# Kernel tuning notes

Measured on AMD Instinct MI355X. Metric: run time of the kernel, lower is better.

Reference implementation:

```python
import jax, jax.numpy as jnp
import numpy as np

N = 100000      # nodes
E = 1600000     # edges
IN, H1, H2, OUT = 128, 128, 64, 128  # layer_channel = [128, (128+128)//2, (128+128)//4, 128]


def setup_inputs() -> dict:
    key = jax.random.key(0)
    ks = jax.random.split(key, 11)
    w = lambda k, s: (jax.random.normal(k, s, jnp.float32) * 0.05)
    return {
        "x": jax.random.normal(ks[0], (N, IN), jnp.float32),
        "edge_index": jax.random.randint(ks[1], (2, E), 0, N),
        "gcn1_w": w(ks[2], (IN, H1)),   "gcn1_b": jnp.zeros((H1,), jnp.float32),
        "fc2_w": w(ks[3], (H1, H1)),   # nn.Linear weight [out, in]
        "gcn3_w": w(ks[4], (H1, H2)),   "gcn3_b": jnp.zeros((H2,), jnp.float32),
        "fc4_w": w(ks[5], (H2, H2)),
        "gcn5_w": w(ks[6], (H2, OUT)),  "gcn5_b": jnp.zeros((OUT,), jnp.float32),
        "fc6_w": w(ks[7], (OUT, OUT)),
    }


def _gcn_norm(edge_index):
    # PyG GCNConv default: add self-loops, symmetric normalization D^-1/2 (A+I) D^-1/2
    loop = jnp.arange(N, dtype=edge_index.dtype)
    src = jnp.concatenate([edge_index[0], loop])
    dst = jnp.concatenate([edge_index[1], loop])
    deg = jax.ops.segment_sum(jnp.ones_like(src, jnp.float32), dst, num_segments=N)
    dinv = jnp.where(deg > 0, jax.lax.rsqrt(jnp.maximum(deg, 1.0)), 0.0)
    norm = dinv[src] * dinv[dst]  # [E+N]
    return src, dst, norm


def _gcn_conv(x, W, b, src, dst, norm):
    h = x @ W                              # [N, d_out]
    msg = h[src] * norm[:, None]           # gather + scale over edges
    return jax.ops.segment_sum(msg, dst, num_segments=N) + b


def reference(x, edge_index, gcn1_w, gcn1_b, fc2_w, gcn3_w, gcn3_b, fc4_w, gcn5_w, gcn5_b, fc6_w):
    src, dst, norm = _gcn_norm(edge_index)
    relu = jax.nn.relu
    z1 = relu(_gcn_conv(x, gcn1_w, gcn1_b, src, dst, norm))
    z1 = relu(z1 + z1 @ fc2_w.T)
    z2 = relu(_gcn_conv(z1, gcn3_w, gcn3_b, src, dst, norm))
    z2 = relu(z2 + z2 @ fc4_w.T)
    z3 = relu(_gcn_conv(z2, gcn5_w, gcn5_b, src, dst, norm))
    z3 = relu(z3 + z3 @ fc6_w.T)
    return z3
```

## Files before the change

### kernel.cpp

```cpp
#include <hip/hip_runtime.h>
#include <cstdint>
#include <cstddef>

#define NN 100000
#define NE 1600000
#define NBB 391
#define BSTRIDE 5120

typedef short short8 __attribute__((ext_vector_type(8)));
typedef float floatx4 __attribute__((ext_vector_type(4)));
typedef unsigned short u16;
typedef uint32_t u32;

__device__ __forceinline__ void split_bf16(float f, short& hi, short& lo) {
    union { float f; uint32_t u; } x;
    x.f = f;
    uint32_t uh = x.u + 0x7FFFu + ((x.u >> 16) & 1u);
    hi = (short)(uh >> 16);
    union { uint32_t u; float f; } hf;
    hf.u = (uh >> 16) << 16;
    float r = f - hf.f;
    union { float f; uint32_t u; } y;
    y.f = r;
    uint32_t ul = y.u + 0x7FFFu + ((y.u >> 16) & 1u);
    lo = (short)(ul >> 16);
}

__device__ __forceinline__ u16 f2bf(float f) {
    union { float f; uint32_t u; } x;
    x.f = f;
    uint32_t r = x.u + 0x7FFFu + ((x.u >> 16) & 1u);
    return (u16)(r >> 16);
}

__device__ __forceinline__ float bf2f(u16 h) {
    union { uint32_t u; float f; } x;
    x.u = ((uint32_t)h) << 16;
    return x.f;
}

__device__ __forceinline__ void acc2(uint32_t u, float& a0, float& a1) {
    union { uint32_t u; float f; } lo, hi;
    lo.u = u << 16;
    hi.u = u & 0xFFFF0000u;
    a0 += lo.f;
    a1 += hi.f;
}

struct WDesc {
    const float* W;
    short* fh;
    short* fl;
    int din, dout, transb, base, total;
};
struct WPrepArgs { WDesc d[6]; int* gcur; };

static __global__ void k_wprep(WPrepArgs args) {
    int tid = blockIdx.x * 256 + threadIdx.x;
    if (tid <= NBB) args.gcur[tid] = 0;
#pragma unroll
    for (int i = 0; i < 6; i++) {
        const WDesc& D = args.d[i];
        if (tid >= D.base && tid < D.base + D.total) {
            int local = tid - D.base;
            int lane = local & 63;
            int rest = local >> 6;
            int kst = D.din >> 5;
            int ks = rest % kst;
            int ntile = rest / kst;
            int n = ntile * 16 + (lane & 15);
            int k0 = ks * 32 + (lane >> 4) * 8;
#pragma unroll
            for (int j = 0; j < 8; j++) {
                int k = k0 + j;
                float v = D.transb ? D.W[(size_t)n * D.din + k]
                                   : D.W[(size_t)k * D.dout + n];
                short h, l;
                split_bf16(v, h, l);
                D.fh[(size_t)local * 8 + j] = h;
                D.fl[(size_t)local * 8 + j] = l;
            }
        }
    }
}


static __global__ __launch_bounds__(1024) void k_bscatterF(const int* __restrict__ src,
                                                           const int* __restrict__ dst,
                                                           int* __restrict__ gcur,
                                                           int2* __restrict__ staging) {
    __shared__ int h[NBB + 1];
    __shared__ int base[NBB + 1];
    int t = threadIdx.x;
    for (int i = t; i < NBB; i += 1024) h[i] = 0;
    __syncthreads();
    int e0 = blockIdx.x * 4096;
    int b[4], l[4], sv[4], dv[4];
#pragma unroll
    for (int j = 0; j < 4; j++) {
        int e = e0 + j * 1024 + t;
        b[j] = -1;
        if (e < NE) {
            sv[j] = src[e];
            dv[j] = dst[e];
            b[j] = dv[j] >> 8;
            l[j] = atomicAdd(&h[b[j]], 1);
        }
    }
    __syncthreads();
    for (int i = t; i < NBB; i += 1024)
        if (h[i]) base[i] = atomicAdd(&gcur[i], h[i]);
    __syncthreads();
#pragma unroll
    for (int j = 0; j < 4; j++)
        if (b[j] >= 0)
            staging[(size_t)b[j] * BSTRIDE + base[b[j]] + l[j]] = make_int2(sv[j], dv[j]);
}

static __global__ __launch_bounds__(1024) void k_blocal2(const int2* __restrict__ staging,
                                                         const int* __restrict__ gcur,
                                                         float* __restrict__ dinv,
                                                         int* __restrict__ row_ptr,
                                                         int* __restrict__ row_end) {
    __shared__ int cnt[256];
    __shared__ int sc[256];
    int b = blockIdx.x;
    int t = threadIdx.x;
    if (t < 256) cnt[t] = 0;
    __syncthreads();
    const int n = gcur[b];
    const int base = b * BSTRIDE;
    for (int i = base + t; i < base + n; i += 1024)
        atomicAdd(&cnt[staging[i].y & 255], 1);
    __syncthreads();
    int myc = (t < 256) ? cnt[t] : 0;
    if (t < 256) sc[t] = myc;
    __syncthreads();
    for (int off = 1; off < 256; off <<= 1) {
        int x = 0;
        if (t < 256 && t >= off) x = sc[t - off];
        __syncthreads();
        if (t < 256) sc[t] += x;
        __syncthreads();
    }
    if (t < 256) {
        int node = (b << 8) + t;
        if (node < NN) {
            dinv[node] = rsqrtf((float)(myc + 1));
            int st = base + sc[t] - myc;
            row_ptr[node] = st;
            row_end[node] = st + myc;
        }
    }
}

static __global__ __launch_bounds__(1024) void k_bfill2(const int2* __restrict__ staging,
                                                        const int* __restrict__ gcur,
                                                        const int* __restrict__ row_ptr,
                                                        int* __restrict__ csr_src) {
    __shared__ int cnt[256];
    __shared__ int lrp[256];
    int b = blockIdx.x;
    int t = threadIdx.x;
    if (t < 256) {
        cnt[t] = 0;
        int node = (b << 8) + t;
        lrp[t] = (node < NN) ? row_ptr[node] : 0;
    }
    __syncthreads();
    const int n = gcur[b];
    const int base = b * BSTRIDE;
    for (int i = base + t; i < base + n; i += 1024) {
        int2 ed = staging[i];
        int loc = ed.y & 255;
        int r = atomicAdd(&cnt[loc], 1);
        csr_src[lrp[loc] + r] = ed.x;
    }
}

template <int DIN, int DOUT, int MT, int AMODE, int OMODE, bool RESID, bool BIAS, bool SCALE>
__global__ __launch_bounds__(256, 3) void k_mgemm(const void* __restrict__ Av,
                                                  const short* __restrict__ fh,
                                                  const short* __restrict__ fl,
                                                  const float* __restrict__ bias,
                                                  const float* __restrict__ dinv,
                                                  void* __restrict__ C) {
    static_assert(!RESID || DIN == DOUT, "residual needs square");
    constexpr int KST = DIN / 32;
    constexpr int NTW = DOUT / 64;
    const int t = threadIdx.x;
    const int wave = t >> 6;
    const int lane = t & 63;
    const int r16 = lane & 15;
    const int kq = lane >> 4;

    const float* Af = (const float*)Av;
    const u16*   Ah = (const u16*)Av;
    const u16*   Al = Ah + (size_t)NN * DIN;

    short8 bh[NTW][KST], bl[NTW][KST];
#pragma unroll
    for (int nt = 0; nt < NTW; nt++) {
        int ntile = wave * NTW + nt;
#pragma unroll
        for (int ks = 0; ks < KST; ks++) {
            size_t o = ((size_t)(ntile * KST + ks) * 64 + lane) * 8;
            bh[nt][ks] = *(const short8*)(fh + o);
            bl[nt][ks] = *(const short8*)(fl + o);
        }
    }

    const int m0b = blockIdx.x * (MT * 16);
#pragma unroll
    for (int mt = 0; mt < MT; mt++) {
        const int m0 = m0b + mt * 16;
        if (m0 >= NN) break;
        const int ra = min(m0 + r16, NN - 1);

        floatx4 acc[NTW];
#pragma unroll
        for (int nt = 0; nt < NTW; nt++) acc[nt] = (floatx4){0.f, 0.f, 0.f, 0.f};

        if constexpr (AMODE == 1) {
            const float* Ap = Af + (size_t)ra * DIN + kq * 8;
#pragma unroll
            for (int ks = 0; ks < KST; ks++) {
                float4 f0 = *(const float4*)(Ap + ks * 32);
                float4 f1 = *(const float4*)(Ap + ks * 32 + 4);
                float fe[8] = {f0.x, f0.y, f0.z, f0.w, f1.x, f1.y, f1.z, f1.w};
                short8 ah;
#pragma unroll
                for (int j = 0; j < 8; j++) ah[j] = (short)f2bf(fe[j]);
#pragma unroll
                for (int nt = 0; nt < NTW; nt++) {
                    acc[nt] = __builtin_amdgcn_mfma_f32_16x16x32_bf16(ah, bh[nt][ks], acc[nt], 0, 0, 0);
                    acc[nt] = __builtin_amdgcn_mfma_f32_16x16x32_bf16(ah, bl[nt][ks], acc[nt], 0, 0, 0);
                }
            }
        } else if constexpr (AMODE == 3) {
            const u16* Aph = Ah + (size_t)ra * DIN + kq * 8;
#pragma unroll
            for (int ks = 0; ks < KST; ks++) {
                short8 ah = *(const short8*)(Aph + ks * 32);
#pragma unroll
                for (int nt = 0; nt < NTW; nt++) {
                    acc[nt] = __builtin_amdgcn_mfma_f32_16x16x32_bf16(ah, bh[nt][ks], acc[nt], 0, 0, 0);
                    acc[nt] = __builtin_amdgcn_mfma_f32_16x16x32_bf16(ah, bl[nt][ks], acc[nt], 0, 0, 0);
                }
            }
        } else {
            const u16* Aph = Ah + (size_t)ra * DIN + kq * 8;
            const u16* Apl = Al + (size_t)ra * DIN + kq * 8;
#pragma unroll
            for (int ks = 0; ks < KST; ks++) {
                short8 ah = *(const short8*)(Aph + ks * 32);
                short8 al = *(const short8*)(Apl + ks * 32);
#pragma unroll
                for (int nt = 0; nt < NTW; nt++) {
                    acc[nt] = __builtin_amdgcn_mfma_f32_16x16x32_bf16(ah, bh[nt][ks], acc[nt], 0, 0, 0);
                    acc[nt] = __builtin_amdgcn_mfma_f32_16x16x32_bf16(ah, bl[nt][ks], acc[nt], 0, 0, 0);
                    acc[nt] = __builtin_amdgcn_mfma_f32_16x16x32_bf16(al, bh[nt][ks], acc[nt], 0, 0, 0);
                }
            }
        }

#pragma unroll
        for (int nt = 0; nt < NTW; nt++) {
            int col = (wave * NTW + nt) * 16 + r16;
#pragma unroll
            for (int r = 0; r < 4; r++) {
                int row = m0 + kq * 4 + r;
                if (row < NN) {
                    float v = acc[nt][r];
                    if constexpr (RESID) {
                        size_t ri = (size_t)row * DIN + col;
                        if constexpr (AMODE == 3)
                            v = fmaxf(v + bf2f(Ah[ri]), 0.f);
                        else
                            v = fmaxf(v + bf2f(Ah[ri]) + bf2f(Al[ri]), 0.f);
                    }
                    if constexpr (BIAS) v = fmaxf(v + bias[col], 0.f);
                    if constexpr (SCALE) v *= dinv[row];
                    size_t oi = (size_t)row * DOUT + col;
                    if constexpr (OMODE == 0) {
                        ((float*)C)[oi] = v;
                    } else if constexpr (OMODE == 1) {
                        ((u16*)C)[oi] = f2bf(v);
                    } else {
                        short h, l;
                        split_bf16(v, h, l);
                        ((u16*)C)[oi] = (u16)h;
                        ((u16*)C)[(size_t)NN * DOUT + oi] = (u16)l;
                    }
                }
            }
        }
    }
}

template <int DIN, int DMID, int DOUT, int MT, bool A1S, bool MIDS, bool RESID1,
          bool BIAS1, bool SCALE2, bool RESID2, int OMODE2>
__global__ __launch_bounds__(256, 3) void k_mfused(const u16* __restrict__ Ahp,
                                                   const short* __restrict__ f1h,
                                                   const short* __restrict__ f1l,
                                                   const short* __restrict__ f2h,
                                                   const short* __restrict__ f2l,
                                                   const float* __restrict__ bias1,
                                                   const float* __restrict__ dinv,
                                                   void* __restrict__ C) {
    static_assert(!RESID1 || DIN == DMID, "resid1 needs square stage1");
    static_assert(!RESID2 || DMID == DOUT, "resid2 needs square stage2");
    constexpr int KST1 = DIN / 32;
    constexpr int NTW1 = DMID / 64;
    constexpr int KST2 = DMID / 32;
    constexpr int NTW2 = DOUT / 64;
    constexpr int LDW = DMID + 8;
    __shared__ u16 ldsh[16][LDW];
    __shared__ u16 ldsl[MIDS ? 1 : 16][LDW];

    const u16* Alp = Ahp + (size_t)NN * DIN;

    const int t = threadIdx.x;
    const int wave = t >> 6;
    const int lane = t & 63;
    const int r16 = lane & 15;
    const int kq = lane >> 4;

    short8 b1h[NTW1][KST1], b1l[NTW1][KST1];
#pragma unroll
    for (int nt = 0; nt < NTW1; nt++) {
        int ntile = wave * NTW1 + nt;
#pragma unroll
        for (int ks = 0; ks < KST1; ks++) {
            size_t o = ((size_t)(ntile * KST1 + ks) * 64 + lane) * 8;
            b1h[nt][ks] = *(const short8*)(f1h + o);
            b1l[nt][ks] = *(const short8*)(f1l + o);
        }
    }
    short8 b2h[NTW2][KST2], b2l[NTW2][KST2];
#pragma unroll
    for (int nt = 0; nt < NTW2; nt++) {
        int ntile = wave * NTW2 + nt;
#pragma unroll
        for (int ks = 0; ks < KST2; ks++) {
            size_t o = ((size_t)(ntile * KST2 + ks) * 64 + lane) * 8;
            b2h[nt][ks] = *(const short8*)(f2h + o);
            b2l[nt][ks] = *(const short8*)(f2l + o);
        }
    }

    const int m0b = blockIdx.x * (MT * 16);
#pragma unroll 1
    for (int mt = 0; mt < MT; mt++) {
        const int m0 = m0b + mt * 16;
        if (m0 >= NN) break;
        const int ra = min(m0 + r16, NN - 1);

        floatx4 acc1[NTW1];
#pragma unroll
        for (int nt = 0; nt < NTW1; nt++) acc1[nt] = (floatx4){0.f, 0.f, 0.f, 0.f};
        {
            const u16* Aph = Ahp + (size_t)ra * DIN + kq * 8;
            const u16* Apl = Alp + (size_t)ra * DIN + kq * 8;
#pragma unroll
            for (int ks = 0; ks < KST1; ks++) {
                short8 ah = *(const short8*)(Aph + ks * 32);
#pragma unroll
                for (int nt = 0; nt < NTW1; nt++) {
                    acc1[nt] = __builtin_amdgcn_mfma_f32_16x16x32_bf16(ah, b1h[nt][ks], acc1[nt], 0, 0, 0);
                    acc1[nt] = __builtin_amdgcn_mfma_f32_16x16x32_bf16(ah, b1l[nt][ks], acc1[nt], 0, 0, 0);
                }
                if constexpr (!A1S) {
                    short8 al = *(const short8*)(Apl + ks * 32);
#pragma unroll
                    for (int nt = 0; nt < NTW1; nt++)
                        acc1[nt] = __builtin_amdgcn_mfma_f32_16x16x32_bf16(al, b1h[nt][ks], acc1[nt], 0, 0, 0);
                }
            }
        }
#pragma unroll
        for (int nt = 0; nt < NTW1; nt++) {
            int col = (wave * NTW1 + nt) * 16 + r16;
#pragma unroll
            for (int r = 0; r < 4; r++) {
                int row = m0 + kq * 4 + r;
                float v = acc1[nt][r];
                if constexpr (RESID1) {
                    if (row < NN) {
                        size_t ri = (size_t)row * DIN + col;
                        if constexpr (A1S)
                            v = fmaxf(v + bf2f(Ahp[ri]), 0.f);
                        else
                            v = fmaxf(v + bf2f(Ahp[ri]) + bf2f(Alp[ri]), 0.f);
                    }
                }
                if constexpr (BIAS1) v = fmaxf(v + bias1[col], 0.f);
                if constexpr (MIDS) {
                    ldsh[kq * 4 + r][col] = f2bf(v);
                } else {
                    short h, l;
                    split_bf16(v, h, l);
                    ldsh[kq * 4 + r][col] = (u16)h;
                    ldsl[kq * 4 + r][col] = (u16)l;
                }
            }
        }
        __syncthreads();

        floatx4 acc2[NTW2];
#pragma unroll
        for (int nt = 0; nt < NTW2; nt++) acc2[nt] = (floatx4){0.f, 0.f, 0.f, 0.f};
#pragma unroll
        for (int ks = 0; ks < KST2; ks++) {
            short8 ah = *(const short8*)&ldsh[r16][ks * 32 + kq * 8];
#pragma unroll
            for (int nt = 0; nt < NTW2; nt++) {
                acc2[nt] = __builtin_amdgcn_mfma_f32_16x16x32_bf16(ah, b2h[nt][ks], acc2[nt], 0, 0, 0);
                acc2[nt] = __builtin_amdgcn_mfma_f32_16x16x32_bf16(ah, b2l[nt][ks], acc2[nt], 0, 0, 0);
            }
            if constexpr (!MIDS) {
                short8 al = *(const short8*)&ldsl[r16][ks * 32 + kq * 8];
#pragma unroll
                for (int nt = 0; nt < NTW2; nt++)
                    acc2[nt] = __builtin_amdgcn_mfma_f32_16x16x32_bf16(al, b2h[nt][ks], acc2[nt], 0, 0, 0);
            }
        }

#pragma unroll
        for (int nt = 0; nt < NTW2; nt++) {
            int col = (wave * NTW2 + nt) * 16 + r16;
#pragma unroll
            for (int r = 0; r < 4; r++) {
                int row = m0 + kq * 4 + r;
                if (row < NN) {
                    float v = acc2[nt][r];
                    if constexpr (RESID2) {
                        if constexpr (MIDS)
                            v = fmaxf(v + bf2f(ldsh[kq * 4 + r][col]), 0.f);
                        else
                            v = fmaxf(v + bf2f(ldsh[kq * 4 + r][col]) + bf2f(ldsl[kq * 4 + r][col]), 0.f);
                    }
                    if constexpr (SCALE2) v *= dinv[row];
                    size_t oi = (size_t)row * DOUT + col;
                    if constexpr (OMODE2 == 0) {
                        ((float*)C)[oi] = v;
                    } else if constexpr (OMODE2 == 1) {
                        ((u16*)C)[oi] = f2bf(v);
                    } else {
                        short h, l;
                        split_bf16(v, h, l);
                        ((u16*)C)[oi] = (u16)h;
                        ((u16*)C)[(size_t)NN * DOUT + oi] = (u16)l;
                    }
                }
            }
        }
        __syncthreads();
    }
}

template <int D, bool BIAS_RELU, int OPL>
__global__ __launch_bounds__(256) void k_agg(const u16* __restrict__ hs,
                                             const float* __restrict__ dinv,
                                             const int* __restrict__ row_ptr,
                                             const int* __restrict__ row_end,
                                             const int* __restrict__ csr_src,
                                             const float* __restrict__ bias,
                                             u16* __restrict__ outh) {
    u16* outl = outh + (size_t)NN * D;
    int node = blockIdx.x * 4 + (threadIdx.x >> 6);
    int lane = threadIdx.x & 63;
    if (node >= NN) return;

    if constexpr (D == 128) {
        const int off = lane * 2;
        float a0 = 0.f, a1 = 0.f;
        {
            uint32_t u = ((const uint32_t*)(hs + (size_t)node * D))[lane];
            acc2(u, a0, a1);
        }
        int e = row_ptr[node];
        const int end = row_end[node];
        for (; e + 16 <= end; e += 16) {
            int s[16];
#pragma unroll
            for (int i = 0; i < 16; i++) s[i] = csr_src[e + i];
            uint32_t v[16];
#pragma unroll
            for (int i = 0; i < 16; i++) v[i] = ((const uint32_t*)(hs + (size_t)s[i] * D))[lane];
#pragma unroll
            for (int i = 0; i < 16; i++) acc2(v[i], a0, a1);
        }
        for (; e + 8 <= end; e += 8) {
            int s[8];
#pragma unroll
            for (int i = 0; i < 8; i++) s[i] = csr_src[e + i];
            uint32_t v[8];
#pragma unroll
            for (int i = 0; i < 8; i++) v[i] = ((const uint32_t*)(hs + (size_t)s[i] * D))[lane];
#pragma unroll
            for (int i = 0; i < 8; i++) acc2(v[i], a0, a1);
        }
        for (; e + 4 <= end; e += 4) {
            int s[4];
#pragma unroll
            for (int i = 0; i < 4; i++) s[i] = csr_src[e + i];
            uint32_t v[4];
#pragma unroll
            for (int i = 0; i < 4; i++) v[i] = ((const uint32_t*)(hs + (size_t)s[i] * D))[lane];
#pragma unroll
            for (int i = 0; i < 4; i++) acc2(v[i], a0, a1);
        }
        for (; e < end; e++) {
            int s = csr_src[e];
            uint32_t u = ((const uint32_t*)(hs + (size_t)s * D))[lane];
            acc2(u, a0, a1);
        }
        const float di = dinv[node];
        a0 *= di;
        a1 *= di;
        if constexpr (BIAS_RELU) {
            a0 = fmaxf(a0 + bias[off], 0.f);
            a1 = fmaxf(a1 + bias[off + 1], 0.f);
        }
        if constexpr (OPL == 1) {
            ushort2 wh;
            wh.x = f2bf(a0); wh.y = f2bf(a1);
            *(ushort2*)(outh + (size_t)node * D + off) = wh;
        } else {
            short h0, l0, h1, l1;
            split_bf16(a0, h0, l0);
            split_bf16(a1, h1, l1);
            ushort2 wh, wl;
            wh.x = (u16)h0; wh.y = (u16)h1;
            wl.x = (u16)l0; wl.y = (u16)l1;
            *(ushort2*)(outh + (size_t)node * D + off) = wh;
            *(ushort2*)(outl + (size_t)node * D + off) = wl;
        }
    } else {
        const int half = lane >> 5;
        const int l32 = lane & 31;
        float a0 = 0.f, a1 = 0.f;
        if (half == 0) {
            uint32_t u = ((const uint32_t*)(hs + (size_t)node * D))[l32];
            acc2(u, a0, a1);
        }
        int e = row_ptr[node];
        const int end = row_end[node];
        for (; e + 16 <= end; e += 16) {
            int s[8];
#pragma unroll
            for (int i = 0; i < 8; i++) s[i] = csr_src[e + half + 2 * i];
            uint32_t v[8];
#pragma unroll
            for (int i = 0; i < 8; i++) v[i] = ((const uint32_t*)(hs + (size_t)s[i] * D))[l32];
#pragma unroll
            for (int i = 0; i < 8; i++) acc2(v[i], a0, a1);
        }
        for (; e + 8 <= end; e += 8) {
            int s[4];
#pragma unroll
            for (int i = 0; i < 4; i++) s[i] = csr_src[e + half + 2 * i];
            uint32_t v[4];
#pragma unroll
            for (int i = 0; i < 4; i++) v[i] = ((const uint32_t*)(hs + (size_t)s[i] * D))[l32];
#pragma unroll
            for (int i = 0; i < 4; i++) acc2(v[i], a0, a1);
        }
        for (; e + 2 <= end; e += 2) {
            int s = csr_src[e + half];
            uint32_t u = ((const uint32_t*)(hs + (size_t)s * D))[l32];
            acc2(u, a0, a1);
        }
        if (e < end && half == 0) {
            int s = csr_src[e];
            uint32_t u = ((const uint32_t*)(hs + (size_t)s * D))[l32];
            acc2(u, a0, a1);
        }
        a0 += __shfl_xor(a0, 32, 64);
        a1 += __shfl_xor(a1, 32, 64);
        if (half == 0) {
            const int off = l32 * 2;
            const float di = dinv[node];
            a0 *= di;
            a1 *= di;
            if constexpr (BIAS_RELU) {
                a0 = fmaxf(a0 + bias[off], 0.f);
                a1 = fmaxf(a1 + bias[off + 1], 0.f);
            }
            if constexpr (OPL == 1) {
                ushort2 wh;
                wh.x = f2bf(a0); wh.y = f2bf(a1);
                *(ushort2*)(outh + (size_t)node * D + off) = wh;
            } else {
                short h0, l0, h1, l1;
                split_bf16(a0, h0, l0);
                split_bf16(a1, h1, l1);
                ushort2 wh, wl;
                wh.x = (u16)h0; wh.y = (u16)h1;
                wl.x = (u16)l0; wl.y = (u16)l1;
                *(ushort2*)(outh + (size_t)node * D + off) = wh;
                *(ushort2*)(outl + (size_t)node * D + off) = wl;
            }
        }
    }
}


extern "C" void kernel_launch(void* const* d_in, const int* in_sizes, int n_in,
                              void* d_out, int out_size, void* d_ws, size_t ws_size,
                              hipStream_t stream) {
    const float* x   = (const float*)d_in[0];
    const int*   ei  = (const int*)d_in[1];
    const float* g1w = (const float*)d_in[2];
    const float* g1b = (const float*)d_in[3];
    const float* f2w = (const float*)d_in[4];
    const float* g3w = (const float*)d_in[5];
    const float* g3b = (const float*)d_in[6];
    const float* f4w = (const float*)d_in[7];
    const float* g5w = (const float*)d_in[8];
    const float* g5b = (const float*)d_in[9];
    const float* f6w = (const float*)d_in[10];
    float* out = (float*)d_out;

    const int* src = ei;
    const int* dst = ei + NE;

    char* p = (char*)d_ws;
    auto alloc = [&](size_t bytes) -> void* {
        void* r = (void*)p;
        p += (bytes + 255) & ~(size_t)255;
        return r;
    };
    float* dinv    = (float*)alloc(NN * 4);
    int*   row_ptr = (int*)alloc(NN * 4);
    int*   row_end = (int*)alloc(NN * 4);
    int*   gcur    = (int*)alloc((NBB + 1) * 4);
    int*   csr     = (int*)alloc((size_t)NBB * BSTRIDE * 4);
    short* wfh     = (short*)alloc(69632 * 2);
    short* wfl     = (short*)alloc(69632 * 2);
    char* bufA = (char*)alloc((size_t)NN * 128 * 4);
    char* bufB = (char*)alloc((size_t)NN * 128 * 4);
    int2* staging  = (int2*)bufB;

    const int gE4 = (NE + 4095) / 4096;
    const int gA  = NN / 4;
    const int gM  = (NN + 31) / 32;

    {
        WPrepArgs a;
        int  eoff[6] = {0, 16384, 32768, 40960, 45056, 53248};
        int  base[6] = {0, 2048, 4096, 5120, 5632, 6656};
        int  tot[6]  = {2048, 2048, 1024, 512, 1024, 2048};
        const float* Ws[6] = {g1w, f2w, g3w, f4w, g5w, f6w};
        int din[6]  = {128, 128, 128, 64, 64, 128};
        int dout[6] = {128, 128, 64, 64, 128, 128};
        int trb[6]  = {0, 1, 0, 1, 0, 1};
        for (int i = 0; i < 6; i++) {
            a.d[i] = WDesc{Ws[i], wfh + eoff[i], wfl + eoff[i],
                           din[i], dout[i], trb[i], base[i], tot[i]};
        }
        a.gcur = gcur;
        k_wprep<<<(8704 + 255) / 256, 256, 0, stream>>>(a);
    }

    k_bscatterF<<<gE4, 1024, 0, stream>>>(src, dst, gcur, staging);
    k_blocal2<<<NBB, 1024, 0, stream>>>(staging, gcur, dinv, row_ptr, row_end);
    k_bfill2<<<NBB, 1024, 0, stream>>>(staging, gcur, row_ptr, csr);

    k_mgemm<128, 128, 2, 1, 1, false, false, true><<<gM, 256, 0, stream>>>(
        x, wfh + 0, wfl + 0, nullptr, dinv, bufA);
    k_agg<128, true, 1><<<gA, 256, 0, stream>>>((const u16*)bufA, dinv, row_ptr, row_end, csr, g1b, (u16*)bufB);
    k_mfused<128, 128, 64, 2, true, true, true, false, true, false, 1><<<gM, 256, 0, stream>>>(
        (const u16*)bufB, wfh + 16384, wfl + 16384, wfh + 32768, wfl + 32768,
        nullptr, dinv, bufA);
    k_agg<64, true, 1><<<gA, 256, 0, stream>>>((const u16*)bufA, dinv, row_ptr, row_end, csr, g3b, (u16*)bufB);
    k_mgemm<64, 64, 2, 3, 1, true, false, true><<<gM, 256, 0, stream>>>(
        bufB, wfh + 40960, wfl + 40960, nullptr, dinv, bufA);
    k_agg<64, false, 2><<<gA, 256, 0, stream>>>((const u16*)bufA, dinv, row_ptr, row_end, csr, nullptr, (u16*)bufB);
    k_mfused<64, 128, 128, 2, false, false, false, true, false, true, 0><<<gM, 256, 0, stream>>>(
        (const u16*)bufB, wfh + 45056, wfl + 45056, wfh + 53248, wfl + 53248,
        g5b, nullptr, out);
}
```

Measured before the change: 447.4 us.

## Fuse CSR build kernels, fold weight prep into scatter, use hardware bf16 pack

Merges the local count/scan kernel with the CSR fill kernel so each bucket stays in one block, folds weight preprocessing into the edge-scatter kernel, and zeroes the bucket counters with a memset. Software bf16 rounding is replaced by the v_cvt_pk_bf16_f32 instruction for packing and hi/lo splitting, and the aggregation accumulators become float2 vectors. This removes kernel launches and a second pass over row_ptr, and trims ALU work on conversion. The hardware conversion may round NaN/edge cases differently from the manual code.

```diff
diff --git a/kernel.cpp b/kernel.cpp
--- a/kernel.cpp
+++ b/kernel.cpp
@@ -9,28 +9,19 @@
 
 typedef short short8 __attribute__((ext_vector_type(8)));
 typedef float floatx4 __attribute__((ext_vector_type(4)));
+typedef float floatx2 __attribute__((ext_vector_type(2)));
+typedef uint32_t u32x4 __attribute__((ext_vector_type(4)));
 typedef unsigned short u16;
 typedef uint32_t u32;
 
-__device__ __forceinline__ void split_bf16(float f, short& hi, short& lo) {
-    union { float f; uint32_t u; } x;
-    x.f = f;
-    uint32_t uh = x.u + 0x7FFFu + ((x.u >> 16) & 1u);
-    hi = (short)(uh >> 16);
-    union { uint32_t u; float f; } hf;
-    hf.u = (uh >> 16) << 16;
-    float r = f - hf.f;
-    union { float f; uint32_t u; } y;
-    y.f = r;
-    uint32_t ul = y.u + 0x7FFFu + ((y.u >> 16) & 1u);
-    lo = (short)(ul >> 16);
+__device__ __forceinline__ u32 cvtpk_bf16(float a, float b) {
+    u32 r;
+    asm("v_cvt_pk_bf16_f32 %0, %1, %2" : "=v"(r) : "v"(a), "v"(b));
+    return r;
 }
 
 __device__ __forceinline__ u16 f2bf(float f) {
-    union { float f; uint32_t u; } x;
-    x.f = f;
-    uint32_t r = x.u + 0x7FFFu + ((x.u >> 16) & 1u);
-    return (u16)(r >> 16);
+    return (u16)(cvtpk_bf16(f, 0.f) & 0xFFFFu);
 }
 
 __device__ __forceinline__ float bf2f(u16 h) {
@@ -39,12 +30,28 @@
     return x.f;
 }
 
-__device__ __forceinline__ void acc2(uint32_t u, float& a0, float& a1) {
+__device__ __forceinline__ void split_bf16(float f, short& hi, short& lo) {
+    u32 h = cvtpk_bf16(f, 0.f) & 0xFFFFu;
+    union { uint32_t u; float f; } hf;
+    hf.u = h << 16;
+    float r = f - hf.f;
+    hi = (short)h;
+    lo = (short)(cvtpk_bf16(r, 0.f) & 0xFFFFu);
+}
+
+__device__ __forceinline__ void split_pair(float a0, float a1, u32& wh, u32& wl) {
+    wh = cvtpk_bf16(a0, a1);
+    union { uint32_t u; float f; } h0, h1;
+    h0.u = wh << 16;
+    h1.u = wh & 0xFFFF0000u;
+    wl = cvtpk_bf16(a0 - h0.f, a1 - h1.f);
+}
+
+__device__ __forceinline__ void acc2v(uint32_t u, floatx2& a) {
     union { uint32_t u; float f; } lo, hi;
     lo.u = u << 16;
     hi.u = u & 0xFFFF0000u;
-    a0 += lo.f;
-    a1 += hi.f;
+    a += (floatx2){lo.f, hi.f};
 }
 
 struct WDesc {
@@ -53,11 +60,9 @@
     short* fl;
     int din, dout, transb, base, total;
 };
-struct WPrepArgs { WDesc d[6]; int* gcur; };
-
-static __global__ void k_wprep(WPrepArgs args) {
-    int tid = blockIdx.x * 256 + threadIdx.x;
-    if (tid <= NBB) args.gcur[tid] = 0;
+struct WPrepArgs { WDesc d[6]; };
+
+__device__ __forceinline__ void wprep_work(const WPrepArgs& args, int tid) {
 #pragma unroll
     for (int i = 0; i < 6; i++) {
         const WDesc& D = args.d[i];
@@ -84,14 +89,20 @@
     }
 }
 
-
-static __global__ __launch_bounds__(1024) void k_bscatterF(const int* __restrict__ src,
-                                                           const int* __restrict__ dst,
-                                                           int* __restrict__ gcur,
-                                                           int2* __restrict__ staging) {
+struct ScatArgs {
+    const int* src;
+    const int* dst;
+    int* gcur;
+    int2* staging;
+    WPrepArgs wp;
+};
+
+static __global__ __launch_bounds__(1024) void k_bscatterF(ScatArgs a) {
     __shared__ int h[NBB + 1];
     __shared__ int base[NBB + 1];
     int t = threadIdx.x;
+    int wtid = blockIdx.x * 1024 + t;
+    if (wtid < 8704) wprep_work(a.wp, wtid);
     for (int i = t; i < NBB; i += 1024) h[i] = 0;
     __syncthreads();
     int e0 = blockIdx.x * 4096;
@@ -101,29 +112,31 @@
         int e = e0 + j * 1024 + t;
         b[j] = -1;
         if (e < NE) {
-            sv[j] = src[e];
-            dv[j] = dst[e];
+            sv[j] = a.src[e];
+            dv[j] = a.dst[e];
             b[j] = dv[j] >> 8;
             l[j] = atomicAdd(&h[b[j]], 1);
         }
     }
     __syncthreads();
     for (int i = t; i < NBB; i += 1024)
-        if (h[i]) base[i] = atomicAdd(&gcur[i], h[i]);
+        if (h[i]) base[i] = atomicAdd(&a.gcur[i], h[i]);
     __syncthreads();
 #pragma unroll
     for (int j = 0; j < 4; j++)
         if (b[j] >= 0)
-            staging[(size_t)b[j] * BSTRIDE + base[b[j]] + l[j]] = make_int2(sv[j], dv[j]);
-}
-
-static __global__ __launch_bounds__(1024) void k_blocal2(const int2* __restrict__ staging,
-                                                         const int* __restrict__ gcur,
-                                                         float* __restrict__ dinv,
-                                                         int* __restrict__ row_ptr,
-                                                         int* __restrict__ row_end) {
+            a.staging[(size_t)b[j] * BSTRIDE + base[b[j]] + l[j]] = make_int2(sv[j], dv[j]);
+}
+
+static __global__ __launch_bounds__(1024) void k_bprep(const int2* __restrict__ staging,
+                                                       const int* __restrict__ gcur,
+                                                       float* __restrict__ dinv,
+                                                       int* __restrict__ row_ptr,
+                                                       int* __restrict__ row_end,
+                                                       int* __restrict__ csr_src) {
     __shared__ int cnt[256];
     __shared__ int sc[256];
+    __shared__ int lrp[256];
     int b = blockIdx.x;
     int t = threadIdx.x;
     if (t < 256) cnt[t] = 0;
@@ -144,32 +157,17 @@
         __syncthreads();
     }
     if (t < 256) {
+        int st = base + sc[t] - myc;
+        lrp[t] = st;
+        cnt[t] = 0;
         int node = (b << 8) + t;
         if (node < NN) {
             dinv[node] = rsqrtf((float)(myc + 1));
-            int st = base + sc[t] - myc;
             row_ptr[node] = st;
             row_end[node] = st + myc;
         }
     }
-}
-
-static __global__ __launch_bounds__(1024) void k_bfill2(const int2* __restrict__ staging,
-                                                        const int* __restrict__ gcur,
-                                                        const int* __restrict__ row_ptr,
-                                                        int* __restrict__ csr_src) {
-    __shared__ int cnt[256];
-    __shared__ int lrp[256];
-    int b = blockIdx.x;
-    int t = threadIdx.x;
-    if (t < 256) {
-        cnt[t] = 0;
-        int node = (b << 8) + t;
-        lrp[t] = (node < NN) ? row_ptr[node] : 0;
-    }
     __syncthreads();
-    const int n = gcur[b];
-    const int base = b * BSTRIDE;
     for (int i = base + t; i < base + n; i += 1024) {
         int2 ed = staging[i];
         int loc = ed.y & 255;
@@ -227,10 +225,12 @@
             for (int ks = 0; ks < KST; ks++) {
                 float4 f0 = *(const float4*)(Ap + ks * 32);
                 float4 f1 = *(const float4*)(Ap + ks * 32 + 4);
-                float fe[8] = {f0.x, f0.y, f0.z, f0.w, f1.x, f1.y, f1.z, f1.w};
-                short8 ah;
-#pragma unroll
-                for (int j = 0; j < 8; j++) ah[j] = (short)f2bf(fe[j]);
+                u32x4 w;
+                w[0] = cvtpk_bf16(f0.x, f0.y);
+                w[1] = cvtpk_bf16(f0.z, f0.w);
+                w[2] = cvtpk_bf16(f1.x, f1.y);
+                w[3] = cvtpk_bf16(f1.z, f1.w);
+                short8 ah = *(const short8*)&w;
 #pragma unroll
                 for (int nt = 0; nt < NTW; nt++) {
                     acc[nt] = __builtin_amdgcn_mfma_f32_16x16x32_bf16(ah, bh[nt][ks], acc[nt], 0, 0, 0);
@@ -474,10 +474,10 @@
 
     if constexpr (D == 128) {
         const int off = lane * 2;
-        float a0 = 0.f, a1 = 0.f;
+        floatx2 a = (floatx2){0.f, 0.f};
         {
             uint32_t u = ((const uint32_t*)(hs + (size_t)node * D))[lane];
-            acc2(u, a0, a1);
+            acc2v(u, a);
         }
         int e = row_ptr[node];
         const int end = row_end[node];
@@ -489,7 +489,7 @@
 #pragma unroll
             for (int i = 0; i < 16; i++) v[i] = ((const uint32_t*)(hs + (size_t)s[i] * D))[lane];
 #pragma unroll
-            for (int i = 0; i < 16; i++) acc2(v[i], a0, a1);
+            for (int i = 0; i < 16; i++) acc2v(v[i], a);
         }
         for (; e + 8 <= end; e += 8) {
             int s[8];
@@ -499,7 +499,7 @@
 #pragma unroll
             for (int i = 0; i < 8; i++) v[i] = ((const uint32_t*)(hs + (size_t)s[i] * D))[lane];
 #pragma unroll
-            for (int i = 0; i < 8; i++) acc2(v[i], a0, a1);
+            for (int i = 0; i < 8; i++) acc2v(v[i], a);
         }
         for (; e + 4 <= end; e += 4) {
             int s[4];
@@ -509,41 +509,34 @@
 #pragma unroll
             for (int i = 0; i < 4; i++) v[i] = ((const uint32_t*)(hs + (size_t)s[i] * D))[lane];
 #pragma unroll
-            for (int i = 0; i < 4; i++) acc2(v[i], a0, a1);
+            for (int i = 0; i < 4; i++) acc2v(v[i], a);
         }
         for (; e < end; e++) {
             int s = csr_src[e];
             uint32_t u = ((const uint32_t*)(hs + (size_t)s * D))[lane];
-            acc2(u, a0, a1);
+            acc2v(u, a);
         }
         const float di = dinv[node];
-        a0 *= di;
-        a1 *= di;
+        float a0 = a[0] * di, a1 = a[1] * di;
         if constexpr (BIAS_RELU) {
             a0 = fmaxf(a0 + bias[off], 0.f);
             a1 = fmaxf(a1 + bias[off + 1], 0.f);
         }
         if constexpr (OPL == 1) {
-            ushort2 wh;
-            wh.x = f2bf(a0); wh.y = f2bf(a1);
-            *(ushort2*)(outh + (size_t)node * D + off) = wh;
+            *(u32*)(outh + (size_t)node * D + off) = cvtpk_bf16(a0, a1);
         } else {
-            short h0, l0, h1, l1;
-            split_bf16(a0, h0, l0);
-            split_bf16(a1, h1, l1);
-            ushort2 wh, wl;
-            wh.x = (u16)h0; wh.y = (u16)h1;
-            wl.x = (u16)l0; wl.y = (u16)l1;
-            *(ushort2*)(outh + (size_t)node * D + off) = wh;
-            *(ushort2*)(outl + (size_t)node * D + off) = wl;
+            u32 wh, wl;
+            split_pair(a0, a1, wh, wl);
+            *(u32*)(outh + (size_t)node * D + off) = wh;
+            *(u32*)(outl + (size_t)node * D + off) = wl;
         }
     } else {
         const int half = lane >> 5;
         const int l32 = lane & 31;
-        float a0 = 0.f, a1 = 0.f;
+        floatx2 a = (floatx2){0.f, 0.f};
         if (half == 0) {
             uint32_t u = ((const uint32_t*)(hs + (size_t)node * D))[l32];
-            acc2(u, a0, a1);
+            acc2v(u, a);
         }
         int e = row_ptr[node];
         const int end = row_end[node];
@@ -555,7 +548,7 @@
 #pragma unroll
             for (int i = 0; i < 8; i++) v[i] = ((const uint32_t*)(hs + (size_t)s[i] * D))[l32];
 #pragma unroll
-            for (int i = 0; i < 8; i++) acc2(v[i], a0, a1);
+            for (int i = 0; i < 8; i++) acc2v(v[i], a);
         }
         for (; e + 8 <= end; e += 8) {
             int s[4];
@@ -565,18 +558,19 @@
 #pragma unroll
             for (int i = 0; i < 4; i++) v[i] = ((const uint32_t*)(hs + (size_t)s[i] * D))[l32];
 #pragma unroll
-            for (int i = 0; i < 4; i++) acc2(v[i], a0, a1);
+            for (int i = 0; i < 4; i++) acc2v(v[i], a);
         }
         for (; e + 2 <= end; e += 2) {
             int s = csr_src[e + half];
             uint32_t u = ((const uint32_t*)(hs + (size_t)s * D))[l32];
-            acc2(u, a0, a1);
+            acc2v(u, a);
         }
         if (e < end && half == 0) {
             int s = csr_src[e];
             uint32_t u = ((const uint32_t*)(hs + (size_t)s * D))[l32];
-            acc2(u, a0, a1);
-        }
+            acc2v(u, a);
+        }
+        float a0 = a[0], a1 = a[1];
         a0 += __shfl_xor(a0, 32, 64);
         a1 += __shfl_xor(a1, 32, 64);
         if (half == 0) {
@@ -589,18 +583,12 @@
                 a1 = fmaxf(a1 + bias[off + 1], 0.f);
             }
             if constexpr (OPL == 1) {
-                ushort2 wh;
-                wh.x = f2bf(a0); wh.y = f2bf(a1);
-                *(ushort2*)(outh + (size_t)node * D + off) = wh;
+                *(u32*)(outh + (size_t)node * D + off) = cvtpk_bf16(a0, a1);
             } else {
-                short h0, l0, h1, l1;
-                split_bf16(a0, h0, l0);
-                split_bf16(a1, h1, l1);
-                ushort2 wh, wl;
-                wh.x = (u16)h0; wh.y = (u16)h1;
-                wl.x = (u16)l0; wl.y = (u16)l1;
-                *(ushort2*)(outh + (size_t)node * D + off) = wh;
-                *(ushort2*)(outl + (size_t)node * D + off) = wl;
+                u32 wh, wl;
+                split_pair(a0, a1, wh, wl);
+                *(u32*)(outh + (size_t)node * D + off) = wh;
+                *(u32*)(outl + (size_t)node * D + off) = wl;
             }
         }
     }
@@ -647,8 +635,14 @@
     const int gA  = NN / 4;
     const int gM  = (NN + 31) / 32;
 
+    hipMemsetAsync(gcur, 0, (NBB + 1) * 4, stream);
+
     {
-        WPrepArgs a;
+        ScatArgs sa;
+        sa.src = src;
+        sa.dst = dst;
+        sa.gcur = gcur;
+        sa.staging = staging;
         int  eoff[6] = {0, 16384, 32768, 40960, 45056, 53248};
         int  base[6] = {0, 2048, 4096, 5120, 5632, 6656};
         int  tot[6]  = {2048, 2048, 1024, 512, 1024, 2048};
@@ -657,16 +651,13 @@
         int dout[6] = {128, 128, 64, 64, 128, 128};
         int trb[6]  = {0, 1, 0, 1, 0, 1};
         for (int i = 0; i < 6; i++) {
-            a.d[i] = WDesc{Ws[i], wfh + eoff[i], wfl + eoff[i],
-                           din[i], dout[i], trb[i], base[i], tot[i]};
-        }
-        a.gcur = gcur;
-        k_wprep<<<(8704 + 255) / 256, 256, 0, stream>>>(a);
-    }
-
-    k_bscatterF<<<gE4, 1024, 0, stream>>>(src, dst, gcur, staging);
-    k_blocal2<<<NBB, 1024, 0, stream>>>(staging, gcur, dinv, row_ptr, row_end);
-    k_bfill2<<<NBB, 1024, 0, stream>>>(staging, gcur, row_ptr, csr);
+            sa.wp.d[i] = WDesc{Ws[i], wfh + eoff[i], wfl + eoff[i],
+                               din[i], dout[i], trb[i], base[i], tot[i]};
+        }
+        k_bscatterF<<<gE4, 1024, 0, stream>>>(sa);
+    }
+
+    k_bprep<<<NBB, 1024, 0, stream>>>(staging, gcur, dinv, row_ptr, row_end, csr);
 
     k_mgemm<128, 128, 2, 1, 1, false, false, true><<<gM, 256, 0, stream>>>(
         x, wfh + 0, wfl + 0, nullptr, dinv, bufA);
```

New measurement: 444.2 us. About the same (-0.7%).
